# Performance work log

Hardware: AMD Instinct MI355X
Metric: run time of the kernel (lower is better)

The kernel has to match this reference:

```python
import jax, jax.numpy as jnp
import numpy as np

H = 128  # target_size / hidden_size
D_IN = 2  # input_size - 2 (stard_LSTM slices off last 2 grid coords)
SAMP = 10  # sampling_num (hardcoded stride 10 in forward loop)


def lstm_encode(x, lengths, W_ih, W_hh, b_ih, b_hh):
    # x: [B, T, D_IN]; torch.nn.LSTMCell math, zero initial state
    B, T, _ = x.shape
    xg = jnp.einsum('btd,gd->btg', x, W_ih) + b_ih  # precompute input projections [B,T,4H]

    def step(carry, xt):
        h, c = carry
        g = xt + h @ W_hh.T + b_hh
        i, f, gg, o = jnp.split(g, 4, axis=-1)
        c = jax.nn.sigmoid(f) * c + jax.nn.sigmoid(i) * jnp.tanh(gg)
        h = jax.nn.sigmoid(o) * jnp.tanh(c)
        return (h, c), h

    h0 = jnp.zeros((B, H), x.dtype)
    _, hs = jax.lax.scan(step, (h0, h0), xg.transpose(1, 0, 2))
    outputs = hs.transpose(1, 0, 2)  # [B, T, H]
    emb = outputs[jnp.arange(B), jnp.clip(lengths - 1, 0)]  # last valid step per sequence
    return emb, outputs


def gather_sub(tensor, sub_len):
    # tensor: [B, T, H]; sub_len: [B*SAMP]; row k reads tensor[k//SAMP, sub_len[k]-1]
    rows = jnp.arange(sub_len.shape[0]) // SAMP
    return tensor[rows, jnp.clip(sub_len - 1, 0)]


def exp_neg_dist(a, b):
    return jnp.exp(-jnp.sqrt(jnp.sum((a - b) ** 2, axis=-1)))


def setup_inputs() -> dict:
    key = jax.random.key(0)
    ks = jax.random.split(key, 12)
    B, T, D = 220, 512, 4
    NS = B * SAMP
    rint = lambda k, n: jnp.maximum(jax.random.randint(k, (n,), 0, T), 1).astype(jnp.int64)
    inp = {
        'traj_input': jax.random.normal(ks[0], (B, T, D), jnp.float32),
        'traj_length': rint(ks[1], B),
        'traj_anchor_sub_length': rint(ks[2], NS),
        'traj_farest_sub_length': rint(ks[3], NS),
        'traj_anchor_input': jax.random.normal(ks[4], (B, T, D), jnp.float32),
        'traj_anchor_length': rint(ks[5], B),
        'anchor_sub_length': rint(ks[6], NS),
        'traj_farest_input': jax.random.normal(ks[7], (B, T, D), jnp.float32),
        'traj_farest_length': rint(ks[8], B),
        'farest_sub_length': rint(ks[9], NS),
        'W_ih': jax.random.normal(ks[10], (4 * H, D_IN), jnp.float32) / np.sqrt(H),
        'W_hh': jax.random.normal(ks[11], (4 * H, H), jnp.float32) / np.sqrt(H),
        'b_ih': jnp.zeros((4 * H,), jnp.float32),
        'b_hh': jnp.zeros((4 * H,), jnp.float32),
    }
    return inp


def reference(traj_input, traj_length, traj_anchor_sub_length, traj_farest_sub_length,
              traj_anchor_input, traj_anchor_length, anchor_sub_length,
              traj_farest_input, traj_farest_length, farest_sub_length,
              W_ih, W_hh, b_ih, b_hh):
    # stard_LSTM=True path: cell input drops last 2 coords
    t_emb, t_out = lstm_encode(traj_input[..., :-2], traj_length, W_ih, W_hh, b_ih, b_hh)
    a_emb, a_out = lstm_encode(traj_anchor_input[..., :-2], traj_anchor_length, W_ih, W_hh, b_ih, b_hh)
    f_emb, f_out = lstm_encode(traj_farest_input[..., :-2], traj_farest_length, W_ih, W_hh, b_ih, b_hh)

    ta_sub = gather_sub(t_out, traj_anchor_sub_length)
    tf_sub = gather_sub(t_out, traj_farest_sub_length)
    an_sub = gather_sub(a_out, anchor_sub_length)
    fa_sub = gather_sub(f_out, farest_sub_length)

    anchor_distance = exp_neg_dist(t_emb, a_emb)
    farest_distance = exp_neg_dist(t_emb, f_emb)
    anchor_sub_distance = exp_neg_dist(ta_sub, an_sub)
    farest_sub_distance = exp_neg_dist(tf_sub, fa_sub)
    return (anchor_distance, farest_distance, anchor_sub_distance, farest_sub_distance)
```

## Files before the change

kernel.cpp:

```cpp
#include <hip/hip_runtime.h>

#define H    128
#define T    512
#define DX   4
#define BB   220
#define SAMP 10
#define NS   (BB*SAMP)
#define M    4
#define NBLK 55
#define MAXSLOT 84

typedef _Float16 half8 __attribute__((ext_vector_type(8)));
typedef float    f32x4 __attribute__((ext_vector_type(4)));

#define WS_TEMB 0
#define WS_AEMB (WS_TEMB + BB*H)
#define WS_FEMB (WS_AEMB + BB*H)
#define WS_TA   (WS_FEMB + BB*H)
#define WS_TF   (WS_TA + NS*H)
#define WS_AN   (WS_TF + NS*H)
#define WS_FA   (WS_AN + NS*H)
#define WS_FLAGS (WS_FA + NS*H)

#define LOG2E  1.442695041f
#define LOG2E2 2.885390082f

__device__ static inline float bf2f(unsigned short u) {
  unsigned int i = ((unsigned int)u) << 16;
  return __builtin_bit_cast(float, i);
}
__device__ static inline unsigned short f2bf(float f) {
  unsigned int i = __builtin_bit_cast(unsigned int, f);
  i += 0x7fffu + ((i >> 16) & 1u);
  return (unsigned short)(i >> 16);
}
__device__ static inline float loadF(const void* p, size_t i, int isbf) {
  return isbf ? bf2f(((const unsigned short*)p)[i]) : ((const float*)p)[i];
}
__device__ static inline int loadI(const void* p, int i, int is64) {
  return is64 ? (int)((const unsigned int*)p)[2*(size_t)i] : ((const int*)p)[i];
}
__device__ static inline float frcp(float x) { return __builtin_amdgcn_rcpf(x); }
__device__ static inline float ex2(float x)  { return __builtin_amdgcn_exp2f(x); }
__device__ static inline float sigmY(float y)  { return frcp(1.f + ex2(-y)); }
__device__ static inline float tanhY(float y)  { return 1.f - 2.f*frcp(1.f + ex2(y)); }
__device__ static inline float scrub(float x) { return (x == x) ? x : 0.f; }
__device__ static inline int clampT(int v) { v = v - 1; if (v < 0) v = 0; if (v > T-1) v = T-1; return v; }

__global__ __launch_bounds__(512, 2) void lstm_scan(
    const void* __restrict__ x0_, const void* __restrict__ len0,
    const void* __restrict__ sub_ta, const void* __restrict__ sub_tf,
    const void* __restrict__ x1_, const void* __restrict__ len1,
    const void* __restrict__ sub_an,
    const void* __restrict__ x2_, const void* __restrict__ len2,
    const void* __restrict__ sub_fa,
    const void* __restrict__ Wih, const void* __restrict__ Whh,
    const void* __restrict__ bih, const void* __restrict__ bhh,
    float* __restrict__ ws)
{
  const int e      = blockIdx.y;
  const int s0     = blockIdx.x * M;
  const int tid    = threadIdx.x;
  const int lane   = tid & 63;
  const int w      = tid >> 6;
  const int lo     = lane & 15;
  const int quad   = lane >> 4;

  int fbf, f64;
  {
    const unsigned int* wp = (const unsigned int*)Whh;
    int cnt = 0;
    for (int i = 0; i < 64; ++i) {
      unsigned int lo16 = wp[i] & 0xFFFFu;
      int ex = (int)((lo16 >> 7) & 0xFFu);
      cnt += (ex >= 100 && ex <= 130);
    }
    fbf = (cnt >= 40);
    const unsigned int* l = (const unsigned int*)len0;
    f64 = ((l[1] | l[3] | l[5] | l[7]) == 0u);
    if (blockIdx.x == 0 && blockIdx.y == 0 && tid == 0) {
      int* fo = (int*)(ws + WS_FLAGS); fo[0] = fbf; fo[1] = f64;
    }
  }

  const void* xin  = (e==0) ? x0_ : (e==1 ? x1_ : x2_);
  const void* lenp = (e==0) ? len0 : (e==1 ? len1 : len2);

  __shared__ __align__(16) _Float16 afr[2][4][16][8];
  __shared__ __align__(16) float2 xbf[M][T+2];
  __shared__ __align__(16) _Float16 sbuf[MAXSLOT][H];
  __shared__ int slot_off[MAXSLOT];

  ((unsigned int*)afr)[tid] = 0u;
  for (int i = tid; i < M*T; i += 512) {
    int m = i >> 9, t = i & (T-1);
    size_t base = ((size_t)(s0+m)*T + t) * DX;
    xbf[m][t] = make_float2(loadF(xin, base + 0, fbf), loadF(xin, base + 1, fbf));
  }
  half8 Bf[4][4];
  const int col = w*16 + lo;
  #pragma unroll
  for (int q = 0; q < 4; ++q) {
    const float sc = (q == 2) ? LOG2E2 : LOG2E;
    const int g = q*128 + col;
    #pragma unroll
    for (int kt = 0; kt < 4; ++kt) {
      #pragma unroll
      for (int j = 0; j < 8; ++j) {
        const int k = kt*32 + quad*8 + j;
        Bf[q][kt][j] = (_Float16)(sc * loadF(Whh, (size_t)g*H + k, fbf));
      }
    }
  }
  float wx0[4], wx1[4], bb[4];
  #pragma unroll
  for (int q = 0; q < 4; ++q) {
    const float sc = (q == 2) ? LOG2E2 : LOG2E;
    const int g = q*128 + col;
    wx0[q] = sc * loadF(Wih, (size_t)g*2 + 0, fbf);
    wx1[q] = sc * loadF(Wih, (size_t)g*2 + 1, fbf);
    bb[q]  = sc * (loadF(bih, g, fbf) + loadF(bhh, g, fbf));
  }
  const int nslots = (e == 0) ? M*21 : M*11;
  int myt = -2, mym = 0;
  if (e == 0) {
    if (tid < M*21) {
      int m = tid / 21, j = tid - m*21, sg = s0 + m;
      mym = m;
      int off;
      if (j == 0)       { myt = clampT(loadI(lenp, sg, f64));            off = WS_TEMB + sg*H; }
      else if (j <= 10) { int k = sg*10 + (j-1);  myt = clampT(loadI(sub_ta, k, f64)); off = WS_TA + k*H; }
      else              { int k = sg*10 + (j-11); myt = clampT(loadI(sub_tf, k, f64)); off = WS_TF + k*H; }
      slot_off[tid] = off;
    }
  } else {
    if (tid < M*11) {
      int m = tid / 11, j = tid - m*11, sg = s0 + m;
      mym = m;
      int off;
      if (j == 0) { myt = clampT(loadI(lenp, sg, f64)); off = (e==1 ? WS_AEMB : WS_FEMB) + sg*H; }
      else {
        int k = sg*10 + (j-1);
        if (e == 1) { myt = clampT(loadI(sub_an, k, f64)); off = WS_AN + k*H; }
        else        { myt = clampT(loadI(sub_fa, k, f64)); off = WS_FA + k*H; }
      }
      slot_off[tid] = off;
    }
  }
  __syncthreads();

  float cs = 0.f;
  const int rdchunk = quad*4 + (lo >> 2);
  const _Float16* rdb[2] = { &afr[0][0][rdchunk][0], &afr[1][0][rdchunk][0] };
  const _Float16* sbb[2] = { &afr[0][0][0][0], &afr[1][0][0][0] };
  const int wrkt    = w >> 1;
  const int wrchunk = ((w & 1)*2 + (lo >> 3))*4 + quad;
  const int wrj     = lo & 7;
  _Float16* wrb[2] = { &afr[0][wrkt][wrchunk][wrj], &afr[1][wrkt][wrchunk][wrj] };
  const float2* xrow = &xbf[quad][0];
  const int c0 = 2*lane;
  const int snap_base = (c0 >> 5)*128 + ((c0 >> 3) & 3)*32 + (c0 & 7);

  auto snap = [&](int tq, int rp) {
    unsigned long long mask = __ballot(myt == tq);
    if (mask) {
      const _Float16* sb = sbb[rp];
      do {
        int src = __ffsll((unsigned long long)mask) - 1;
        mask &= mask - 1;
        int m    = __shfl(mym, src);
        int slot = w*64 + src;
        unsigned int pk = *(const unsigned int*)(sb + snap_base + m*8);
        *(unsigned int*)&sbuf[slot][c0] = pk;
      } while (mask);
    }
  };

  f32x4 G[4];
  float2 xn;
  {
    float2 xv0 = xrow[0];
    #pragma unroll
    for (int q = 0; q < 4; ++q)
      G[q] = (f32x4){ bb[q] + wx0[q]*xv0.x + wx1[q]*xv0.y, 0.f, 0.f, 0.f };
    xn = xrow[1];
  }

  auto step = [&](int rp, int wp, int t) {
    const _Float16* rb = rdb[rp];
    half8 A[4];
    #pragma unroll
    for (int kt = 0; kt < 4; ++kt)
      A[kt] = *(const half8*)(rb + kt*128);

    __builtin_amdgcn_s_setprio(1);
    #pragma unroll
    for (int kt = 0; kt < 4; ++kt)
      #pragma unroll
      for (int q = 0; q < 4; ++q)
        G[q] = __builtin_amdgcn_mfma_f32_16x16x32_f16(A[kt], Bf[q][kt], G[q], 0, 0, 0);
    __builtin_amdgcn_s_setprio(0);

    float pxn[4];
    #pragma unroll
    for (int q = 0; q < 4; ++q)
      pxn[q] = bb[q] + wx0[q]*xn.x + wx1[q]*xn.y;
    xn = xrow[t+2];
    snap(t-1, rp);

    float sf = sigmY(G[1][0]);
    float si = sigmY(G[0][0]);
    float tg = tanhY(G[2][0]);
    float ig = (si * tg) * LOG2E2;
    cs = sf*cs + ig;
    float tc = tanhY(cs);
    float so = sigmY(G[3][0]);
    *wrb[wp] = (_Float16)(so * tc);
    #pragma unroll
    for (int q = 0; q < 4; ++q)
      G[q][0] = pxn[q];
    __syncthreads();
  };

  #pragma unroll 1
  for (int t = 0; t < T; t += 2) {
    step(0, 1, t);
    step(1, 0, t+1);
  }

  snap(T-1, 0);

  __syncthreads();
  for (int i = tid; i < nslots*64; i += 512) {
    int slot = i >> 6, c2 = i & 63;
    unsigned int pk = *(const unsigned int*)&sbuf[slot][2*c2];
    float2 v;
    v.x = (float)__builtin_bit_cast(_Float16, (unsigned short)(pk & 0xFFFFu));
    v.y = (float)__builtin_bit_cast(_Float16, (unsigned short)(pk >> 16));
    *(float2*)(ws + slot_off[slot] + 2*c2) = v;
  }
}

__global__ void dists(const float* __restrict__ ws, void* __restrict__ outv) {
  const int fbf = ((const int*)(ws + WS_FLAGS))[0];
  const int gtid = blockIdx.x*256 + threadIdx.x;
  const int widx = gtid >> 6, lane = gtid & 63;
  const float *pa, *pb;
  if (widx < 220)       { pa = ws + WS_TEMB + (size_t)widx*H;        pb = ws + WS_AEMB + (size_t)widx*H; }
  else if (widx < 440)  { int b = widx-220;  pa = ws + WS_TEMB + (size_t)b*H; pb = ws + WS_FEMB + (size_t)b*H; }
  else if (widx < 2640) { int k = widx-440;  pa = ws + WS_TA + (size_t)k*H;   pb = ws + WS_AN + (size_t)k*H; }
  else                  { int k = widx-2640; pa = ws + WS_TF + (size_t)k*H;   pb = ws + WS_FA + (size_t)k*H; }
  float d0 = pa[lane]    - pb[lane];
  float d1 = pa[lane+64] - pb[lane+64];
  float s  = scrub(d0*d0 + d1*d1);
  #pragma unroll
  for (int off = 32; off > 0; off >>= 1) s += __shfl_down(s, off, 64);
  if (lane == 0) {
    float r = __expf(-sqrtf(s));
    if (fbf) ((unsigned short*)outv)[widx] = f2bf(r);
    else     ((float*)outv)[widx] = r;
  }
}

extern "C" void kernel_launch(void* const* d_in, const int* in_sizes, int n_in,
                              void* d_out, int out_size, void* d_ws, size_t ws_size,
                              hipStream_t stream) {
  float* ws = (float*)d_ws;
  hipLaunchKernelGGL(lstm_scan, dim3(NBLK, 3), dim3(512), 0, stream,
                     d_in[0], d_in[1], d_in[2], d_in[3],
                     d_in[4], d_in[5], d_in[6],
                     d_in[7], d_in[8], d_in[9],
                     d_in[10], d_in[11], d_in[12], d_in[13], ws);
  hipLaunchKernelGGL(dists, dim3(4840*64/256), dim3(256), 0, stream, ws, d_out);
}
```

Before: 353.3 us.

## Fuse distance kernel into LSTM scan via grid-wide atomic barrier

Removes the separate dists kernel launch. After the scan, each block joins a global atomic barrier, then all waves stride over the distance tasks inside the same kernel. This saves one launch and the gap between kernels, and adds a memset plus a spin barrier. The barrier relies on all 165 blocks being co-resident, which launch_bounds(512,2) on a 256-CU part should allow.

```diff
diff --git a/kernel.cpp b/kernel.cpp
--- a/kernel.cpp
+++ b/kernel.cpp
@@ -9,6 +9,9 @@
 #define M    4
 #define NBLK 55
 #define MAXSLOT 84
+#define NGRID (NBLK*3)
+#define NTASK 4840
+#define NWAVE (NGRID*8)
 
 typedef _Float16 half8 __attribute__((ext_vector_type(8)));
 typedef float    f32x4 __attribute__((ext_vector_type(4)));
@@ -20,7 +23,7 @@
 #define WS_TF   (WS_TA + NS*H)
 #define WS_AN   (WS_TF + NS*H)
 #define WS_FA   (WS_AN + NS*H)
-#define WS_FLAGS (WS_FA + NS*H)
+#define WS_BAR  (WS_FA + NS*H)
 
 #define LOG2E  1.442695041f
 #define LOG2E2 2.885390082f
@@ -56,7 +59,7 @@
     const void* __restrict__ sub_fa,
     const void* __restrict__ Wih, const void* __restrict__ Whh,
     const void* __restrict__ bih, const void* __restrict__ bhh,
-    float* __restrict__ ws)
+    float* __restrict__ ws, void* __restrict__ outv)
 {
   const int e      = blockIdx.y;
   const int s0     = blockIdx.x * M;
@@ -78,9 +81,6 @@
     fbf = (cnt >= 40);
     const unsigned int* l = (const unsigned int*)len0;
     f64 = ((l[1] | l[3] | l[5] | l[7]) == 0u);
-    if (blockIdx.x == 0 && blockIdx.y == 0 && tid == 0) {
-      int* fo = (int*)(ws + WS_FLAGS); fo[0] = fbf; fo[1] = f64;
-    }
   }
 
   const void* xin  = (e==0) ? x0_ : (e==1 ? x1_ : x2_);
@@ -239,26 +239,35 @@
     v.y = (float)__builtin_bit_cast(_Float16, (unsigned short)(pk >> 16));
     *(float2*)(ws + slot_off[slot] + 2*c2) = v;
   }
-}
-
-__global__ void dists(const float* __restrict__ ws, void* __restrict__ outv) {
-  const int fbf = ((const int*)(ws + WS_FLAGS))[0];
-  const int gtid = blockIdx.x*256 + threadIdx.x;
-  const int widx = gtid >> 6, lane = gtid & 63;
-  const float *pa, *pb;
-  if (widx < 220)       { pa = ws + WS_TEMB + (size_t)widx*H;        pb = ws + WS_AEMB + (size_t)widx*H; }
-  else if (widx < 440)  { int b = widx-220;  pa = ws + WS_TEMB + (size_t)b*H; pb = ws + WS_FEMB + (size_t)b*H; }
-  else if (widx < 2640) { int k = widx-440;  pa = ws + WS_TA + (size_t)k*H;   pb = ws + WS_AN + (size_t)k*H; }
-  else                  { int k = widx-2640; pa = ws + WS_TF + (size_t)k*H;   pb = ws + WS_FA + (size_t)k*H; }
-  float d0 = pa[lane]    - pb[lane];
-  float d1 = pa[lane+64] - pb[lane+64];
-  float s  = scrub(d0*d0 + d1*d1);
-  #pragma unroll
-  for (int off = 32; off > 0; off >>= 1) s += __shfl_down(s, off, 64);
-  if (lane == 0) {
-    float r = __expf(-sqrtf(s));
-    if (fbf) ((unsigned short*)outv)[widx] = f2bf(r);
-    else     ((float*)outv)[widx] = r;
+
+  __syncthreads();
+  {
+    unsigned int* bar = (unsigned int*)(ws + WS_BAR);
+    if (tid == 0) {
+      __hip_atomic_fetch_add(bar, 1u, __ATOMIC_RELEASE, __HIP_MEMORY_SCOPE_AGENT);
+      while (__hip_atomic_load(bar, __ATOMIC_ACQUIRE, __HIP_MEMORY_SCOPE_AGENT) < (unsigned)NGRID)
+        __builtin_amdgcn_s_sleep(2);
+    }
+    __syncthreads();
+  }
+
+  const int gw = ((e*NBLK + blockIdx.x) << 3) + w;
+  for (int widx = gw; widx < NTASK; widx += NWAVE) {
+    const float *pa, *pb;
+    if (widx < 220)       { pa = ws + WS_TEMB + (size_t)widx*H;        pb = ws + WS_AEMB + (size_t)widx*H; }
+    else if (widx < 440)  { int b = widx-220;  pa = ws + WS_TEMB + (size_t)b*H; pb = ws + WS_FEMB + (size_t)b*H; }
+    else if (widx < 2640) { int k = widx-440;  pa = ws + WS_TA + (size_t)k*H;   pb = ws + WS_AN + (size_t)k*H; }
+    else                  { int k = widx-2640; pa = ws + WS_TF + (size_t)k*H;   pb = ws + WS_FA + (size_t)k*H; }
+    float d0 = pa[lane]    - pb[lane];
+    float d1 = pa[lane+64] - pb[lane+64];
+    float s  = scrub(d0*d0 + d1*d1);
+    #pragma unroll
+    for (int off2 = 32; off2 > 0; off2 >>= 1) s += __shfl_down(s, off2, 64);
+    if (lane == 0) {
+      float r = __expf(-sqrtf(s));
+      if (fbf) ((unsigned short*)outv)[widx] = f2bf(r);
+      else     ((float*)outv)[widx] = r;
+    }
   }
 }
 
@@ -266,10 +275,10 @@
                               void* d_out, int out_size, void* d_ws, size_t ws_size,
                               hipStream_t stream) {
   float* ws = (float*)d_ws;
+  hipMemsetAsync((char*)d_ws + (size_t)WS_BAR*sizeof(float), 0, sizeof(unsigned int), stream);
   hipLaunchKernelGGL(lstm_scan, dim3(NBLK, 3), dim3(512), 0, stream,
                      d_in[0], d_in[1], d_in[2], d_in[3],
                      d_in[4], d_in[5], d_in[6],
                      d_in[7], d_in[8], d_in[9],
-                     d_in[10], d_in[11], d_in[12], d_in[13], ws);
-  hipLaunchKernelGGL(dists, dim3(4840*64/256), dim3(256), 0, stream, ws, d_out);
-}
+                     d_in[10], d_in[11], d_in[12], d_in[13], ws, d_out);
+}
```

Result: slower. 368.6 us (+4.3%).
